# Performance work log

Hardware: AMD Instinct MI355X
Metric: run time of the kernel (lower is better)

The kernel has to match this reference:

```python
import jax, jax.numpy as jnp
import numpy as np

D_MODEL = 1024
NUM_HEADS = 16
HEAD_DIM = D_MODEL // NUM_HEADS


def setup_inputs() -> dict:
    key = jax.random.key(0)
    ks = jax.random.split(key, 9)
    B, S = 2, 2048
    s = 1.0 / np.sqrt(D_MODEL)
    inp = {
        "x": jax.random.normal(ks[0], (B, S, D_MODEL), dtype=jnp.float32),
        "Wq": jax.random.normal(ks[1], (D_MODEL, D_MODEL), dtype=jnp.float32) * s,
        "bq": jnp.zeros((D_MODEL,), dtype=jnp.float32),
        "Wk": jax.random.normal(ks[2], (D_MODEL, D_MODEL), dtype=jnp.float32) * s,
        "bk": jnp.zeros((D_MODEL,), dtype=jnp.float32),
        "Wv": jax.random.normal(ks[3], (D_MODEL, D_MODEL), dtype=jnp.float32) * s,
        "bv": jnp.zeros((D_MODEL,), dtype=jnp.float32),
        "Wo": jax.random.normal(ks[4], (D_MODEL, D_MODEL), dtype=jnp.float32) * s,
        "bo": jnp.zeros((D_MODEL,), dtype=jnp.float32),
    }
    return inp


def _rope(x, seq_len):
    # x: [B, H, S, Dh]; rotate-half RoPE with base 10000
    dh = x.shape[-1]
    inv_freq = 1.0 / (10000.0 ** (jnp.arange(0, dh, 2, dtype=jnp.float32) / dh))
    t = jnp.arange(seq_len, dtype=jnp.float32)
    freqs = jnp.einsum("i,j->ij", t, inv_freq)          # [S, Dh/2]
    emb = jnp.concatenate([freqs, freqs], axis=-1)        # [S, Dh]
    cos = jnp.cos(emb)[None, None, :, :]
    sin = jnp.sin(emb)[None, None, :, :]
    x1, x2 = jnp.split(x, 2, axis=-1)
    rot = jnp.concatenate([-x2, x1], axis=-1)
    return x * cos + rot * sin


def reference(x, Wq, bq, Wk, bk, Wv, bv, Wo, bo):
    B, S, _ = x.shape
    H, Dh = NUM_HEADS, HEAD_DIM

    def proj(W, b):
        y = x @ W.T + b                                   # [B, S, D]
        return y.reshape(B, S, H, Dh).transpose(0, 2, 1, 3)  # [B, H, S, Dh]

    q = _rope(proj(Wq, bq), S)
    k = _rope(proj(Wk, bk), S)
    v = proj(Wv, bv)

    scores = jnp.einsum("bhqd,bhkd->bhqk", q, k) / jnp.sqrt(jnp.float32(Dh))
    causal = jnp.triu(jnp.ones((S, S), dtype=bool), k=1)  # True above diag -> masked
    scores = jnp.where(causal[None, None], -jnp.inf, scores)
    attn = jax.nn.softmax(scores, axis=-1)
    out = jnp.einsum("bhqk,bhkd->bhqd", attn, v)          # [B, H, S, Dh]
    out = out.transpose(0, 2, 1, 3).reshape(B, S, H * Dh)
    return out @ Wo.T + bo
```

## Files before the change

### kernel.cpp

```cpp
#include <hip/hip_runtime.h>
#include <math.h>

typedef __bf16 bf16_t;
typedef bf16_t bf16x8 __attribute__((ext_vector_type(8)));
typedef float f32x4 __attribute__((ext_vector_type(4)));

#define S_LEN 2048
#define NHEAD 16
#define DHEAD 64
#define DMODEL 1024
#define BATCH 2

__device__ __forceinline__ float bf2f(unsigned short u) {
    unsigned int x = ((unsigned int)u) << 16;
    return __builtin_bit_cast(float, x);
}
__device__ __forceinline__ unsigned short f2bf(float f) {
    unsigned int x = __builtin_bit_cast(unsigned int, f);
    x += 0x7fffu + ((x >> 16) & 1u);
    return (unsigned short)(x >> 16);
}

__device__ __forceinline__ void glds16(const void* g, void* l) {
    __builtin_amdgcn_global_load_lds(
        (__attribute__((address_space(1))) void*)g,
        (__attribute__((address_space(3))) void*)l,
        16, 0, 0);
}

#define SCALE2 0.1803368801f

__global__ __launch_bounds__(256) void cvt_kernel(
    const float* __restrict__ x,  const float* __restrict__ wq,
    const float* __restrict__ wk, const float* __restrict__ wv,
    const float* __restrict__ wo,
    unsigned short* __restrict__ xb,  unsigned short* __restrict__ wqb,
    unsigned short* __restrict__ wkb, unsigned short* __restrict__ wvb,
    unsigned short* __restrict__ wob)
{
    const int y = blockIdx.y;
    const float* s = (y == 0) ? x : (y == 1) ? wq : (y == 2) ? wk : (y == 3) ? wv : wo;
    unsigned short* d = (y == 0) ? xb : (y == 1) ? wqb : (y == 2) ? wkb : (y == 3) ? wvb : wob;
    const int n4 = (y == 0) ? (1 << 20) : (1 << 18);
    const int i = blockIdx.x * 256 + threadIdx.x;
    if (i < n4) {
        float4 v = ((const float4*)s)[i];
        ushort4 o;
        o.x = f2bf(v.x); o.y = f2bf(v.y); o.z = f2bf(v.z); o.w = f2bf(v.w);
        ((ushort4*)d)[i] = o;
    }
}

__global__ __launch_bounds__(256) void rope_table_kernel(float2* __restrict__ tab)
{
    const int gid = blockIdx.x * 256 + threadIdx.x;
    const int s = gid >> 5, d = gid & 31;
    const float freq = exp2f(-0.4152410119f * (float)d);
    const float ang = (float)s * freq;
    tab[gid] = make_float2(cosf(ang), sinf(ang));
}

__global__ __launch_bounds__(256, 2) void qkv_gemm_kernel(
    const unsigned short* __restrict__ xb,
    const unsigned short* __restrict__ wqb, const unsigned short* __restrict__ wkb,
    const unsigned short* __restrict__ wvb,
    const float* __restrict__ bq, const float* __restrict__ bk, const float* __restrict__ bv,
    const float2* __restrict__ tab,
    unsigned short* __restrict__ Qr, unsigned short* __restrict__ Kr,
    unsigned short* __restrict__ VT)
{
    __shared__ __align__(16) unsigned short As[128 * 32];
    __shared__ __align__(16) unsigned short Bs[128 * 32];

    const int which = blockIdx.x >> 3;
    const int bn = (blockIdx.x & 7) * 128;
    const int bm = blockIdx.y * 128;
    const unsigned short* W = (which == 0) ? wqb : (which == 1) ? wkb : wvb;
    const float* bias       = (which == 0) ? bq  : (which == 1) ? bk  : bv;

    const int tid  = threadIdx.x;
    const int lane = tid & 63;
    const int w    = tid >> 6;
    const int quad = lane >> 4;
    const int l16  = lane & 15;
    const int wm   = (w >> 1) * 64;
    const int wn   = (w & 1) * 64;

    f32x4 acc[4][4];
#pragma unroll
    for (int i = 0; i < 4; ++i)
#pragma unroll
        for (int j = 0; j < 4; ++j)
            acc[i][j] = f32x4{0.f, 0.f, 0.f, 0.f};

    const int r0 = tid >> 2, c0 = (tid & 3) * 8;
    const unsigned short* ga0 = xb + (size_t)(bm + r0) * DMODEL + c0;
    const unsigned short* ga1 = ga0 + (size_t)64 * DMODEL;
    const unsigned short* gb0 = W  + (size_t)(bn + r0) * DMODEL + c0;
    const unsigned short* gb1 = gb0 + (size_t)64 * DMODEL;
    unsigned short* la0 = As + tid * 8;
    unsigned short* la1 = As + (tid + 256) * 8;
    unsigned short* lb0 = Bs + tid * 8;
    unsigned short* lb1 = Bs + (tid + 256) * 8;

    for (int k0 = 0; k0 < DMODEL; k0 += 32) {
        glds16(ga0 + k0, la0);
        glds16(ga1 + k0, la1);
        glds16(gb0 + k0, lb0);
        glds16(gb1 + k0, lb1);
        __syncthreads();

        bf16x8 aF[4], bF[4];
#pragma unroll
        for (int t = 0; t < 4; ++t) {
            aF[t] = *(const bf16x8*)(&As[(wm + t * 16 + l16) * 32 + quad * 8]);
            bF[t] = *(const bf16x8*)(&Bs[(wn + t * 16 + l16) * 32 + quad * 8]);
        }
#pragma unroll
        for (int mt = 0; mt < 4; ++mt)
#pragma unroll
            for (int nt = 0; nt < 4; ++nt)
                acc[mt][nt] = __builtin_amdgcn_mfma_f32_16x16x32_bf16(
                    aF[mt], bF[nt], acc[mt][nt], 0, 0, 0);
        __syncthreads();
    }

    if (which < 2) {
        unsigned short* Y = (which == 0) ? Qr : Kr;
        const float qscale = (which == 0) ? SCALE2 : 1.0f;
#pragma unroll
        for (int mt = 0; mt < 4; ++mt) {
            const int row0 = bm + wm + mt * 16 + quad * 4;
#pragma unroll
            for (int nt = 0; nt < 2; ++nt) {
                const int d   = nt * 16 + l16;
                const int col = bn + wn + nt * 16 + l16;
                const float b1 = bias[col];
                const float b2 = bias[col + 32];
#pragma unroll
                for (int r = 0; r < 4; ++r) {
                    const int row = row0 + r;
                    const int s = row & (S_LEN - 1);
                    const float2 cs = tab[s * 32 + d];
                    const float x1 = acc[mt][nt][r] + b1;
                    const float x2 = acc[mt][nt + 2][r] + b2;
                    Y[(size_t)row * DMODEL + col]      = f2bf((x1 * cs.x - x2 * cs.y) * qscale);
                    Y[(size_t)row * DMODEL + col + 32] = f2bf((x2 * cs.x + x1 * cs.y) * qscale);
                }
            }
        }
    } else {
#pragma unroll
        for (int mt = 0; mt < 4; ++mt) {
            const int row0 = bm + wm + mt * 16 + quad * 4;
            const int bb = row0 >> 11, s0 = row0 & (S_LEN - 1);
            const int h = (bn + wn) >> 6;
#pragma unroll
            for (int nt = 0; nt < 4; ++nt) {
                const int d = nt * 16 + l16;
                const float bv2 = bias[bn + wn + nt * 16 + l16];
                unsigned short pk[4];
#pragma unroll
                for (int r = 0; r < 4; ++r)
                    pk[r] = f2bf(acc[mt][nt][r] + bv2);
                *(uint2*)(&VT[((size_t)(bb * NHEAD + h) * DHEAD + d) * S_LEN + s0]) =
                    *(const uint2*)pk;
            }
        }
    }
}

#define VSTR 136

__global__ __launch_bounds__(512, 4) void attn_kernel(
    const unsigned short* __restrict__ Q, const unsigned short* __restrict__ K,
    const unsigned short* __restrict__ VT, unsigned short* __restrict__ O)
{
    const int j  = blockIdx.x;
    const int u  = j & 255;
    const int b  = j >> 8;
    const int m  = u & 15;
    int qt = (m & 1) ? (m >> 1) : (15 - (m >> 1));
    if (b) qt = 15 - qt;
    const int h  = u >> 4;

    const int tid  = threadIdx.x;
    const int w    = tid >> 6;
    const int lane = tid & 63;
    const int quad = lane >> 4;
    const int l16  = lane & 15;

    __shared__ __align__(16) unsigned short Ks[128 * 64];
    __shared__ __align__(16) unsigned short Vt[64 * 128];
    __shared__ __align__(16) unsigned short Pb[8 * 16 * VSTR];

    const int q0 = qt * 128;
    const unsigned short* Qb = Q  + (size_t)b * S_LEN * DMODEL + h * DHEAD;
    const unsigned short* Kb = K  + (size_t)b * S_LEN * DMODEL + h * DHEAD;
    const unsigned short* Vh = VT + ((size_t)(b * NHEAD + h)) * DHEAD * S_LEN;

    const int qrow = q0 + w * 16 + l16;
    const bf16x8 qf0 = *(const bf16x8*)(Qb + (size_t)qrow * DMODEL + quad * 8);
    const bf16x8 qf1 = *(const bf16x8*)(Qb + (size_t)qrow * DMODEL + 32 + quad * 8);

    f32x4 o[4];
#pragma unroll
    for (int i = 0; i < 4; ++i) o[i] = f32x4{0.f, 0.f, 0.f, 0.f};
    float l_i[4] = {0.f, 0.f, 0.f, 0.f};

    const int nkt = qt + 1;
    unsigned short* Pw = &Pb[w * 16 * VSTR];

    for (int kt = 0; kt < nkt; ++kt) {
#pragma unroll
        for (int i = 0; i < 2; ++i) {
            const int ck = tid + i * 512;
            const int krow = ck >> 3, kc = ck & 7;
            glds16(Kb + (size_t)(kt * 128 + krow) * DMODEL + ((kc ^ (krow & 7)) * 8),
                   Ks + ck * 8);
            const int vrow = ck >> 4, vc = ck & 15;
            glds16(Vh + (size_t)vrow * S_LEN + kt * 128 + ((vc ^ (vrow & 15)) * 8),
                   Vt + ck * 8);
        }
        __syncthreads();

        const bool diag = (kt == nkt - 1);
        const int ntmax = diag ? ((w & ~1) + 2) : 8;
        const int cmax  = ntmax >> 1;

        f32x4 sc[8];
#pragma unroll
        for (int nt = 0; nt < 8; ++nt) {
            if (nt >= ntmax) break;
            const int row = nt * 16 + l16;
            const bf16x8 kf0 = *(const bf16x8*)(&Ks[row * 64 + ((quad ^ (l16 & 7)) * 8)]);
            const bf16x8 kf1 = *(const bf16x8*)(&Ks[row * 64 + (((4 + quad) ^ (l16 & 7)) * 8)]);
            f32x4 a = f32x4{0.f, 0.f, 0.f, 0.f};
            a = __builtin_amdgcn_mfma_f32_16x16x32_bf16(qf0, kf0, a, 0, 0, 0);
            a = __builtin_amdgcn_mfma_f32_16x16x32_bf16(qf1, kf1, a, 0, 0, 0);
            sc[nt] = a;
        }

        if (diag) {
            const int qpos0 = q0 + w * 16 + quad * 4;
#pragma unroll
            for (int nt = 0; nt < 8; ++nt) {
                if (nt >= ntmax) break;
                const int kpos = kt * 128 + nt * 16 + l16;
#pragma unroll
                for (int r = 0; r < 4; ++r)
                    if (kpos > qpos0 + r) sc[nt][r] = -INFINITY;
            }
        }

#pragma unroll
        for (int nt = 0; nt < 8; ++nt) {
            if (nt >= ntmax) break;
#pragma unroll
            for (int r = 0; r < 4; ++r) {
                const float e = exp2f(sc[nt][r]);
                sc[nt][r] = e;
                l_i[r] += e;
            }
        }

#pragma unroll
        for (int nt = 0; nt < 8; ++nt) {
            if (nt >= ntmax) break;
#pragma unroll
            for (int r = 0; r < 4; ++r)
                Pw[(quad * 4 + r) * VSTR + nt * 16 + l16] = f2bf(sc[nt][r]);
        }

        bf16x8 pA[4];
#pragma unroll
        for (int c = 0; c < 4; ++c) {
            if (c >= cmax) break;
            pA[c] = *(const bf16x8*)(&Pw[l16 * VSTR + c * 32 + quad * 8]);
        }
#pragma unroll
        for (int nt = 0; nt < 4; ++nt) {
            const int row = nt * 16 + l16;
#pragma unroll
            for (int c = 0; c < 4; ++c) {
                if (c >= cmax) break;
                const bf16x8 vF = *(const bf16x8*)(&Vt[row * 128 + (((c * 4 + quad) ^ l16) * 8)]);
                o[nt] = __builtin_amdgcn_mfma_f32_16x16x32_bf16(pA[c], vF, o[nt], 0, 0, 0);
            }
        }
        __syncthreads();
    }

    float linv[4];
#pragma unroll
    for (int r = 0; r < 4; ++r) {
        float rs = l_i[r];
#pragma unroll
        for (int msk = 1; msk < 16; msk <<= 1)
            rs += __shfl_xor(rs, msk);
        linv[r] = 1.0f / rs;
    }
    const int spos0 = q0 + w * 16 + quad * 4;
#pragma unroll
    for (int nt = 0; nt < 4; ++nt)
#pragma unroll
        for (int r = 0; r < 4; ++r) {
            const float val = o[nt][r] * linv[r];
            O[((size_t)b * S_LEN + spos0 + r) * DMODEL + h * DHEAD + nt * 16 + l16] = f2bf(val);
        }
}

__global__ __launch_bounds__(256, 2) void outproj_kernel(
    const unsigned short* __restrict__ A, const unsigned short* __restrict__ W,
    const float* __restrict__ bias, float* __restrict__ C)
{
    __shared__ __align__(16) unsigned short As[64 * 32];
    __shared__ __align__(16) unsigned short Bs[128 * 32];

    const int tid  = threadIdx.x;
    const int lane = tid & 63;
    const int w    = tid >> 6;
    const int quad = lane >> 4;
    const int l16  = lane & 15;
    const int wm   = (w >> 1) * 32;
    const int wn   = (w & 1) * 64;
    const int bm   = blockIdx.y * 64;
    const int bn   = blockIdx.x * 128;

    f32x4 acc[2][4];
#pragma unroll
    for (int i = 0; i < 2; ++i)
#pragma unroll
        for (int j = 0; j < 4; ++j)
            acc[i][j] = f32x4{0.f, 0.f, 0.f, 0.f};

    const int r0 = tid >> 2, c0 = (tid & 3) * 8;
    const unsigned short* ga  = A + (size_t)(bm + r0) * DMODEL + c0;
    const unsigned short* gb0 = W + (size_t)(bn + r0) * DMODEL + c0;
    const unsigned short* gb1 = gb0 + (size_t)64 * DMODEL;
    unsigned short* la  = As + tid * 8;
    unsigned short* lb0 = Bs + tid * 8;
    unsigned short* lb1 = Bs + (tid + 256) * 8;

    for (int k0 = 0; k0 < DMODEL; k0 += 32) {
        glds16(ga + k0, la);
        glds16(gb0 + k0, lb0);
        glds16(gb1 + k0, lb1);
        __syncthreads();

        bf16x8 aF[2], bF[4];
#pragma unroll
        for (int t = 0; t < 2; ++t)
            aF[t] = *(const bf16x8*)(&As[(wm + t * 16 + l16) * 32 + quad * 8]);
#pragma unroll
        for (int t = 0; t < 4; ++t)
            bF[t] = *(const bf16x8*)(&Bs[(wn + t * 16 + l16) * 32 + quad * 8]);
#pragma unroll
        for (int mt = 0; mt < 2; ++mt)
#pragma unroll
            for (int nt = 0; nt < 4; ++nt)
                acc[mt][nt] = __builtin_amdgcn_mfma_f32_16x16x32_bf16(
                    aF[mt], bF[nt], acc[mt][nt], 0, 0, 0);
        __syncthreads();
    }

#pragma unroll
    for (int mt = 0; mt < 2; ++mt) {
        const int row0 = bm + wm + mt * 16 + quad * 4;
#pragma unroll
        for (int nt = 0; nt < 4; ++nt) {
            const int col = bn + wn + nt * 16 + l16;
            const float bv = bias[col];
#pragma unroll
            for (int r = 0; r < 4; ++r)
                C[(size_t)(row0 + r) * DMODEL + col] = acc[mt][nt][r] + bv;
        }
    }
}

extern "C" void kernel_launch(void* const* d_in, const int* in_sizes, int n_in,
                              void* d_out, int out_size, void* d_ws, size_t ws_size,
                              hipStream_t stream) {
    const float* x  = (const float*)d_in[0];
    const float* Wq = (const float*)d_in[1];
    const float* bq = (const float*)d_in[2];
    const float* Wk = (const float*)d_in[3];
    const float* bk = (const float*)d_in[4];
    const float* Wv = (const float*)d_in[5];
    const float* bv = (const float*)d_in[6];
    const float* Wo = (const float*)d_in[7];
    const float* bo = (const float*)d_in[8];
    float* out = (float*)d_out;

    char* ws = (char*)d_ws;
    const size_t MB = 1 << 20;
    unsigned short* xb  = (unsigned short*)(ws);
    unsigned short* wqb = (unsigned short*)(ws + 8  * MB);
    unsigned short* wkb = (unsigned short*)(ws + 10 * MB);
    unsigned short* wvb = (unsigned short*)(ws + 12 * MB);
    unsigned short* wob = (unsigned short*)(ws + 14 * MB);
    float2*         tab = (float2*)       (ws + 16 * MB);
    unsigned short* Qr  = (unsigned short*)(ws + 17 * MB);
    unsigned short* Kr  = (unsigned short*)(ws + 25 * MB);
    unsigned short* VT  = (unsigned short*)(ws + 33 * MB);
    unsigned short* AO  = (unsigned short*)(ws + 41 * MB);

    const int M = BATCH * S_LEN;

    cvt_kernel<<<dim3(4096, 5), 256, 0, stream>>>(
        x, Wq, Wk, Wv, Wo, xb, wqb, wkb, wvb, wob);

    rope_table_kernel<<<256, 256, 0, stream>>>(tab);

    qkv_gemm_kernel<<<dim3(24, M / 128), 256, 0, stream>>>(
        xb, wqb, wkb, wvb, bq, bk, bv, tab, Qr, Kr, VT);

    attn_kernel<<<dim3(512), 512, 0, stream>>>(Qr, Kr, VT, AO);

    outproj_kernel<<<dim3(DMODEL / 128, M / 64), 256, 0, stream>>>(AO, wob, bo, out);
}
```

Baseline: 198.3 us.

## Split causal attention along KV into chunks and add a combine kernel

The attention kernel now processes at most four KV tiles per block, so the grid grows from 512 to 1280 blocks. Long query tiles are spread over several blocks, which should cut the tail caused by causal imbalance, where the last query tile needs sixteen KV tiles and the first needs one. Each block writes unnormalized fp32 partial outputs and row sums to workspace, and a new combine kernel adds them, normalizes, and writes the bf16 result. The cost is an extra launch and extra global traffic for the fp32 partials. Summing partials directly is only correct because the softmax does not track a per-block running max.

```diff
diff --git a/kernel.cpp b/kernel.cpp
--- a/kernel.cpp
+++ b/kernel.cpp
@@ -171,18 +171,25 @@
 }
 
 #define VSTR 136
+#define CHUNK 4
 
 __global__ __launch_bounds__(512, 4) void attn_kernel(
     const unsigned short* __restrict__ Q, const unsigned short* __restrict__ K,
-    const unsigned short* __restrict__ VT, unsigned short* __restrict__ O)
-{
-    const int j  = blockIdx.x;
-    const int u  = j & 255;
-    const int b  = j >> 8;
-    const int m  = u & 15;
-    int qt = (m & 1) ? (m >> 1) : (15 - (m >> 1));
-    if (b) qt = 15 - qt;
-    const int h  = u >> 4;
+    const unsigned short* __restrict__ VT,
+    float* __restrict__ Opart, float* __restrict__ Lpart)
+{
+    const int j   = blockIdx.x;
+    const int bh  = j / 40;
+    const int cid = 39 - (j - bh * 40);
+    const int b   = bh >> 4, h = bh & 15;
+    int g, rel;
+    if (cid < 4)       { g = 0; rel = cid; }
+    else if (cid < 12) { g = 1; rel = cid - 4; }
+    else if (cid < 24) { g = 2; rel = cid - 12; }
+    else               { g = 3; rel = cid - 24; }
+    const int qt = 4 * g + rel / (g + 1);
+    const int cs = rel - (rel / (g + 1)) * (g + 1);
+    const int slot = bh * 40 + cid;
 
     const int tid  = threadIdx.x;
     const int w    = tid >> 6;
@@ -208,10 +215,11 @@
     for (int i = 0; i < 4; ++i) o[i] = f32x4{0.f, 0.f, 0.f, 0.f};
     float l_i[4] = {0.f, 0.f, 0.f, 0.f};
 
-    const int nkt = qt + 1;
+    const int k0t  = cs * CHUNK;
+    const int kend = (k0t + CHUNK < qt + 1) ? (k0t + CHUNK) : (qt + 1);
     unsigned short* Pw = &Pb[w * 16 * VSTR];
 
-    for (int kt = 0; kt < nkt; ++kt) {
+    for (int kt = k0t; kt < kend; ++kt) {
 #pragma unroll
         for (int i = 0; i < 2; ++i) {
             const int ck = tid + i * 512;
@@ -224,7 +232,7 @@
         }
         __syncthreads();
 
-        const bool diag = (kt == nkt - 1);
+        const bool diag = (kt == qt);
         const int ntmax = diag ? ((w & ~1) + 2) : 8;
         const int cmax  = ntmax >> 1;
 
@@ -291,23 +299,53 @@
         __syncthreads();
     }
 
-    float linv[4];
+    float* Op = Opart + (size_t)slot * (128 * 64);
+    float* Lp = Lpart + slot * 128;
+    const int row0 = w * 16 + quad * 4;
 #pragma unroll
     for (int r = 0; r < 4; ++r) {
         float rs = l_i[r];
 #pragma unroll
         for (int msk = 1; msk < 16; msk <<= 1)
             rs += __shfl_xor(rs, msk);
-        linv[r] = 1.0f / rs;
-    }
-    const int spos0 = q0 + w * 16 + quad * 4;
+        if (l16 == 0) Lp[row0 + r] = rs;
+    }
 #pragma unroll
     for (int nt = 0; nt < 4; ++nt)
 #pragma unroll
-        for (int r = 0; r < 4; ++r) {
-            const float val = o[nt][r] * linv[r];
-            O[((size_t)b * S_LEN + spos0 + r) * DMODEL + h * DHEAD + nt * 16 + l16] = f2bf(val);
-        }
+        for (int r = 0; r < 4; ++r)
+            Op[(row0 + r) * 64 + nt * 16 + l16] = o[nt][r];
+}
+
+__global__ __launch_bounds__(256) void attn_combine_kernel(
+    const float* __restrict__ Opart, const float* __restrict__ Lpart,
+    unsigned short* __restrict__ AO)
+{
+    const int bid = blockIdx.x;
+    const int b = bid >> 8, rem = bid & 255, h = rem >> 4, qt = rem & 15;
+    const int g = qt >> 2, rr = qt & 3;
+    const int off = (g + 1) * (2 * g + rr);
+    const int nc  = g + 1;
+    const int s0  = (b * NHEAD + h) * 40 + off;
+    const int t   = threadIdx.x;
+
+#pragma unroll
+    for (int jj = 0; jj < 8; ++jj) {
+        const int idx = jj * 1024 + t * 4;
+        const int row = idx >> 6, dh = idx & 63;
+        float4 acc = make_float4(0.f, 0.f, 0.f, 0.f);
+        float l = 0.f;
+        for (int c = 0; c < nc; ++c) {
+            const float4 p = *(const float4*)(Opart + (size_t)(s0 + c) * 8192 + idx);
+            acc.x += p.x; acc.y += p.y; acc.z += p.z; acc.w += p.w;
+            l += Lpart[(s0 + c) * 128 + row];
+        }
+        const float linv = 1.0f / l;
+        ushort4 o;
+        o.x = f2bf(acc.x * linv); o.y = f2bf(acc.y * linv);
+        o.z = f2bf(acc.z * linv); o.w = f2bf(acc.w * linv);
+        *(ushort4*)(AO + ((size_t)(b * S_LEN + qt * 128 + row)) * DMODEL + h * DHEAD + dh) = o;
+    }
 }
 
 __global__ __launch_bounds__(256, 2) void outproj_kernel(
@@ -404,6 +442,8 @@
     unsigned short* Kr  = (unsigned short*)(ws + 25 * MB);
     unsigned short* VT  = (unsigned short*)(ws + 33 * MB);
     unsigned short* AO  = (unsigned short*)(ws + 41 * MB);
+    float*          Opart = (float*)      (ws + 49 * MB);
+    float*          Lpart = (float*)      (ws + 90 * MB);
 
     const int M = BATCH * S_LEN;
 
@@ -415,7 +455,9 @@
     qkv_gemm_kernel<<<dim3(24, M / 128), 256, 0, stream>>>(
         xb, wqb, wkb, wvb, bq, bk, bv, tab, Qr, Kr, VT);
 
-    attn_kernel<<<dim3(512), 512, 0, stream>>>(Qr, Kr, VT, AO);
+    attn_kernel<<<dim3(1280), 512, 0, stream>>>(Qr, Kr, VT, Opart, Lpart);
+
+    attn_combine_kernel<<<dim3(512), 256, 0, stream>>>(Opart, Lpart, AO);
 
     outproj_kernel<<<dim3(DMODEL / 128, M / 64), 256, 0, stream>>>(AO, wob, bo, out);
 }
```

After: 227.2 us. 14.6% more time.

## Pair causal query tiles per block and double-buffer K/V loads in attention

Applied to the files above, without the earlier changes.

Each attention block now handles two complementary query tiles (15-m and m), so every block does a balanced 17 key-tile steps, and the grid is halved to 256 blocks. K and V tiles are double-buffered in LDS, with the next tile's async global-to-LDS loads issued before the current tile's compute and gated by explicit vmcnt waits and raw barriers. This targets causal load imbalance and exposed load latency. In exchange it doubles K/V LDS use, drops the occupancy hint, and leaves fewer blocks than the previous 512 to fill the GPU's compute units.

```diff
diff --git a/kernel.cpp b/kernel.cpp
--- a/kernel.cpp
+++ b/kernel.cpp
@@ -171,18 +171,18 @@
 }
 
 #define VSTR 136
-
-__global__ __launch_bounds__(512, 4) void attn_kernel(
+#define NSTG 17
+
+__global__ __launch_bounds__(512) void attn_kernel(
     const unsigned short* __restrict__ Q, const unsigned short* __restrict__ K,
     const unsigned short* __restrict__ VT, unsigned short* __restrict__ O)
 {
-    const int j  = blockIdx.x;
-    const int u  = j & 255;
-    const int b  = j >> 8;
-    const int m  = u & 15;
-    int qt = (m & 1) ? (m >> 1) : (15 - (m >> 1));
-    if (b) qt = 15 - qt;
-    const int h  = u >> 4;
+    const int j   = blockIdx.x;
+    const int bh  = j >> 3;
+    const int m   = j & 7;
+    const int b   = bh >> 4, h = bh & 15;
+    const int qtA = 15 - m;
+    const int nA  = qtA + 1;
 
     const int tid  = threadIdx.x;
     const int w    = tid >> 6;
@@ -190,41 +190,66 @@
     const int quad = lane >> 4;
     const int l16  = lane & 15;
 
-    __shared__ __align__(16) unsigned short Ks[128 * 64];
-    __shared__ __align__(16) unsigned short Vt[64 * 128];
+    __shared__ __align__(16) unsigned short Ks[2][128 * 64];
+    __shared__ __align__(16) unsigned short Vt[2][64 * 128];
     __shared__ __align__(16) unsigned short Pb[8 * 16 * VSTR];
 
-    const int q0 = qt * 128;
     const unsigned short* Qb = Q  + (size_t)b * S_LEN * DMODEL + h * DHEAD;
     const unsigned short* Kb = K  + (size_t)b * S_LEN * DMODEL + h * DHEAD;
     const unsigned short* Vh = VT + ((size_t)(b * NHEAD + h)) * DHEAD * S_LEN;
 
-    const int qrow = q0 + w * 16 + l16;
-    const bf16x8 qf0 = *(const bf16x8*)(Qb + (size_t)qrow * DMODEL + quad * 8);
-    const bf16x8 qf1 = *(const bf16x8*)(Qb + (size_t)qrow * DMODEL + 32 + quad * 8);
+    const int rA = qtA * 128 + w * 16 + l16;
+    const int rB = m   * 128 + w * 16 + l16;
+    const bf16x8 qfA0 = *(const bf16x8*)(Qb + (size_t)rA * DMODEL + quad * 8);
+    const bf16x8 qfA1 = *(const bf16x8*)(Qb + (size_t)rA * DMODEL + 32 + quad * 8);
+    const bf16x8 qfB0 = *(const bf16x8*)(Qb + (size_t)rB * DMODEL + quad * 8);
+    const bf16x8 qfB1 = *(const bf16x8*)(Qb + (size_t)rB * DMODEL + 32 + quad * 8);
 
     f32x4 o[4];
 #pragma unroll
     for (int i = 0; i < 4; ++i) o[i] = f32x4{0.f, 0.f, 0.f, 0.f};
     float l_i[4] = {0.f, 0.f, 0.f, 0.f};
 
-    const int nkt = qt + 1;
     unsigned short* Pw = &Pb[w * 16 * VSTR];
 
-    for (int kt = 0; kt < nkt; ++kt) {
-#pragma unroll
-        for (int i = 0; i < 2; ++i) {
-            const int ck = tid + i * 512;
-            const int krow = ck >> 3, kc = ck & 7;
-            glds16(Kb + (size_t)(kt * 128 + krow) * DMODEL + ((kc ^ (krow & 7)) * 8),
-                   Ks + ck * 8);
-            const int vrow = ck >> 4, vc = ck & 15;
-            glds16(Vh + (size_t)vrow * S_LEN + kt * 128 + ((vc ^ (vrow & 15)) * 8),
-                   Vt + ck * 8);
-        }
-        __syncthreads();
-
-        const bool diag = (kt == nkt - 1);
+#define STAGE(bs, kt_) do {                                                        \
+        _Pragma("unroll")                                                          \
+        for (int i_ = 0; i_ < 2; ++i_) {                                           \
+            const int ck = tid + i_ * 512;                                         \
+            const int krow = ck >> 3, kc = ck & 7;                                 \
+            glds16(Kb + (size_t)((kt_) * 128 + krow) * DMODEL + ((kc ^ (krow & 7)) * 8), \
+                   &Ks[bs][ck * 8]);                                               \
+            const int vrow = ck >> 4, vc = ck & 15;                                \
+            glds16(Vh + (size_t)vrow * S_LEN + (kt_) * 128 + ((vc ^ (vrow & 15)) * 8), \
+                   &Vt[bs][ck * 8]);                                               \
+        }                                                                          \
+    } while (0)
+
+    STAGE(0, 0);
+
+    for (int st = 0; st < NSTG; ++st) {
+        const int cur = st & 1;
+
+        if (st + 1 < NSTG) {
+            const int kt2 = (st + 1 < nA) ? (st + 1) : (st + 1 - nA);
+            STAGE(cur ^ 1, kt2);
+            if (st == nA) {
+                asm volatile("s_waitcnt vmcnt(20)" ::: "memory");
+            } else {
+                asm volatile("s_waitcnt vmcnt(4)" ::: "memory");
+            }
+        } else {
+            asm volatile("s_waitcnt vmcnt(0)" ::: "memory");
+        }
+        __builtin_amdgcn_s_barrier();
+
+        const int inA = (st < nA) ? 1 : 0;
+        const int qt  = inA ? qtA : m;
+        const int kt  = inA ? st : st - nA;
+        const bf16x8 qv0 = inA ? qfA0 : qfB0;
+        const bf16x8 qv1 = inA ? qfA1 : qfB1;
+
+        const bool diag = (kt == qt);
         const int ntmax = diag ? ((w & ~1) + 2) : 8;
         const int cmax  = ntmax >> 1;
 
@@ -233,16 +258,16 @@
         for (int nt = 0; nt < 8; ++nt) {
             if (nt >= ntmax) break;
             const int row = nt * 16 + l16;
-            const bf16x8 kf0 = *(const bf16x8*)(&Ks[row * 64 + ((quad ^ (l16 & 7)) * 8)]);
-            const bf16x8 kf1 = *(const bf16x8*)(&Ks[row * 64 + (((4 + quad) ^ (l16 & 7)) * 8)]);
+            const bf16x8 kf0 = *(const bf16x8*)(&Ks[cur][row * 64 + ((quad ^ (l16 & 7)) * 8)]);
+            const bf16x8 kf1 = *(const bf16x8*)(&Ks[cur][row * 64 + (((4 + quad) ^ (l16 & 7)) * 8)]);
             f32x4 a = f32x4{0.f, 0.f, 0.f, 0.f};
-            a = __builtin_amdgcn_mfma_f32_16x16x32_bf16(qf0, kf0, a, 0, 0, 0);
-            a = __builtin_amdgcn_mfma_f32_16x16x32_bf16(qf1, kf1, a, 0, 0, 0);
+            a = __builtin_amdgcn_mfma_f32_16x16x32_bf16(qv0, kf0, a, 0, 0, 0);
+            a = __builtin_amdgcn_mfma_f32_16x16x32_bf16(qv1, kf1, a, 0, 0, 0);
             sc[nt] = a;
         }
 
         if (diag) {
-            const int qpos0 = q0 + w * 16 + quad * 4;
+            const int qpos0 = qt * 128 + w * 16 + quad * 4;
 #pragma unroll
             for (int nt = 0; nt < 8; ++nt) {
                 if (nt >= ntmax) break;
@@ -284,30 +309,59 @@
 #pragma unroll
             for (int c = 0; c < 4; ++c) {
                 if (c >= cmax) break;
-                const bf16x8 vF = *(const bf16x8*)(&Vt[row * 128 + (((c * 4 + quad) ^ l16) * 8)]);
+                const bf16x8 vF = *(const bf16x8*)(&Vt[cur][row * 128 + (((c * 4 + quad) ^ l16) * 8)]);
                 o[nt] = __builtin_amdgcn_mfma_f32_16x16x32_bf16(pA[c], vF, o[nt], 0, 0, 0);
             }
         }
-        __syncthreads();
-    }
-
-    float linv[4];
-#pragma unroll
-    for (int r = 0; r < 4; ++r) {
-        float rs = l_i[r];
-#pragma unroll
-        for (int msk = 1; msk < 16; msk <<= 1)
-            rs += __shfl_xor(rs, msk);
-        linv[r] = 1.0f / rs;
-    }
-    const int spos0 = q0 + w * 16 + quad * 4;
-#pragma unroll
-    for (int nt = 0; nt < 4; ++nt)
+
+        asm volatile("s_waitcnt lgkmcnt(0)" ::: "memory");
+        __builtin_amdgcn_s_barrier();
+
+        if (st == nA - 1) {
+            float linv[4];
+#pragma unroll
+            for (int r = 0; r < 4; ++r) {
+                float rs = l_i[r];
+#pragma unroll
+                for (int msk = 1; msk < 16; msk <<= 1)
+                    rs += __shfl_xor(rs, msk);
+                linv[r] = 1.0f / rs;
+            }
+            const int spos0 = qtA * 128 + w * 16 + quad * 4;
+#pragma unroll
+            for (int nt = 0; nt < 4; ++nt)
+#pragma unroll
+                for (int r = 0; r < 4; ++r) {
+                    const float val = o[nt][r] * linv[r];
+                    O[((size_t)b * S_LEN + spos0 + r) * DMODEL + h * DHEAD + nt * 16 + l16] = f2bf(val);
+                }
+#pragma unroll
+            for (int i = 0; i < 4; ++i) o[i] = f32x4{0.f, 0.f, 0.f, 0.f};
+#pragma unroll
+            for (int r = 0; r < 4; ++r) l_i[r] = 0.f;
+        }
+    }
+#undef STAGE
+
+    {
+        float linv[4];
 #pragma unroll
         for (int r = 0; r < 4; ++r) {
-            const float val = o[nt][r] * linv[r];
-            O[((size_t)b * S_LEN + spos0 + r) * DMODEL + h * DHEAD + nt * 16 + l16] = f2bf(val);
-        }
+            float rs = l_i[r];
+#pragma unroll
+            for (int msk = 1; msk < 16; msk <<= 1)
+                rs += __shfl_xor(rs, msk);
+            linv[r] = 1.0f / rs;
+        }
+        const int spos0 = m * 128 + w * 16 + quad * 4;
+#pragma unroll
+        for (int nt = 0; nt < 4; ++nt)
+#pragma unroll
+            for (int r = 0; r < 4; ++r) {
+                const float val = o[nt][r] * linv[r];
+                O[((size_t)b * S_LEN + spos0 + r) * DMODEL + h * DHEAD + nt * 16 + l16] = f2bf(val);
+            }
+    }
 }
 
 __global__ __launch_bounds__(256, 2) void outproj_kernel(
@@ -415,7 +469,7 @@
     qkv_gemm_kernel<<<dim3(24, M / 128), 256, 0, stream>>>(
         xb, wqb, wkb, wvb, bq, bk, bv, tab, Qr, Kr, VT);
 
-    attn_kernel<<<dim3(512), 512, 0, stream>>>(Qr, Kr, VT, AO);
+    attn_kernel<<<dim3(256), 512, 0, stream>>>(Qr, Kr, VT, AO);
 
     outproj_kernel<<<dim3(DMODEL / 128, M / 64), 256, 0, stream>>>(AO, wob, bo, out);
 }
```

After: 206.2 us. +4.0%, slower.

## Double-buffer K/V tiles and build P operand in registers via lane shuffles

Applied to the files above, without the earlier changes.

The attention kernel now double-buffers the K and V tiles in LDS, prefetching the next tile with async global-to-LDS loads while the current one is computed, and uses explicit vmcnt waits with raw barriers. The QK MFMA operands are swapped so the score tile is transposed, which lets the P matrix be packed to bf16 with v_cvt_pk_bf16_f32 and rearranged through cross-lane shuffles instead of a round trip through an LDS scratch buffer. The block-to-tile mapping is also reordered to interleave heads with long and short causal tiles. This trades LDS traffic and load latency for extra shuffle and select instructions, and the doubled K/V buffers may change occupancy.

```diff
diff --git a/kernel.cpp b/kernel.cpp
--- a/kernel.cpp
+++ b/kernel.cpp
@@ -4,6 +4,7 @@
 typedef __bf16 bf16_t;
 typedef bf16_t bf16x8 __attribute__((ext_vector_type(8)));
 typedef float f32x4 __attribute__((ext_vector_type(4)));
+typedef unsigned int u32x4 __attribute__((ext_vector_type(4)));
 
 #define S_LEN 2048
 #define NHEAD 16
@@ -170,19 +171,15 @@
     }
 }
 
-#define VSTR 136
-
 __global__ __launch_bounds__(512, 4) void attn_kernel(
     const unsigned short* __restrict__ Q, const unsigned short* __restrict__ K,
     const unsigned short* __restrict__ VT, unsigned short* __restrict__ O)
 {
     const int j  = blockIdx.x;
-    const int u  = j & 255;
-    const int b  = j >> 8;
-    const int m  = u & 15;
-    int qt = (m & 1) ? (m >> 1) : (15 - (m >> 1));
-    if (b) qt = 15 - qt;
-    const int h  = u >> 4;
+    const int bh = j & 31;
+    const int qs = j >> 5;
+    const int b  = bh >> 4, h = bh & 15;
+    const int qt = (qs < 8) ? (15 - qs) : (qs - 8);
 
     const int tid  = threadIdx.x;
     const int w    = tid >> 6;
@@ -190,9 +187,8 @@
     const int quad = lane >> 4;
     const int l16  = lane & 15;
 
-    __shared__ __align__(16) unsigned short Ks[128 * 64];
-    __shared__ __align__(16) unsigned short Vt[64 * 128];
-    __shared__ __align__(16) unsigned short Pb[8 * 16 * VSTR];
+    __shared__ __align__(16) unsigned short Ks[2][128 * 64];
+    __shared__ __align__(16) unsigned short Vt[2][64 * 128];
 
     const int q0 = qt * 128;
     const unsigned short* Qb = Q  + (size_t)b * S_LEN * DMODEL + h * DHEAD;
@@ -206,25 +202,37 @@
     f32x4 o[4];
 #pragma unroll
     for (int i = 0; i < 4; ++i) o[i] = f32x4{0.f, 0.f, 0.f, 0.f};
-    float l_i[4] = {0.f, 0.f, 0.f, 0.f};
+    float l_acc = 0.f;
 
     const int nkt = qt + 1;
-    unsigned short* Pw = &Pb[w * 16 * VSTR];
+
+#define STAGE(bs, kt_) do {                                                        \
+        _Pragma("unroll")                                                          \
+        for (int i_ = 0; i_ < 2; ++i_) {                                           \
+            const int ck = tid + i_ * 512;                                         \
+            const int krow = ck >> 3, kc = ck & 7;                                 \
+            glds16(Kb + (size_t)((kt_) * 128 + krow) * DMODEL + ((kc ^ (krow & 7)) * 8), \
+                   &Ks[bs][ck * 8]);                                               \
+            const int vrow = ck >> 4, vc = ck & 15;                                \
+            glds16(Vh + (size_t)vrow * S_LEN + (kt_) * 128 + ((vc ^ (vrow & 15)) * 8), \
+                   &Vt[bs][ck * 8]);                                               \
+        }                                                                          \
+    } while (0)
+
+    STAGE(0, 0);
 
     for (int kt = 0; kt < nkt; ++kt) {
-#pragma unroll
-        for (int i = 0; i < 2; ++i) {
-            const int ck = tid + i * 512;
-            const int krow = ck >> 3, kc = ck & 7;
-            glds16(Kb + (size_t)(kt * 128 + krow) * DMODEL + ((kc ^ (krow & 7)) * 8),
-                   Ks + ck * 8);
-            const int vrow = ck >> 4, vc = ck & 15;
-            glds16(Vh + (size_t)vrow * S_LEN + kt * 128 + ((vc ^ (vrow & 15)) * 8),
-                   Vt + ck * 8);
-        }
-        __syncthreads();
-
-        const bool diag = (kt == nkt - 1);
+        const int cur = kt & 1;
+
+        if (kt + 1 < nkt) {
+            STAGE(cur ^ 1, kt + 1);
+            asm volatile("s_waitcnt vmcnt(4)" ::: "memory");
+        } else {
+            asm volatile("s_waitcnt vmcnt(0)" ::: "memory");
+        }
+        __builtin_amdgcn_s_barrier();
+
+        const bool diag = (kt == qt);
         const int ntmax = diag ? ((w & ~1) + 2) : 8;
         const int cmax  = ntmax >> 1;
 
@@ -233,23 +241,22 @@
         for (int nt = 0; nt < 8; ++nt) {
             if (nt >= ntmax) break;
             const int row = nt * 16 + l16;
-            const bf16x8 kf0 = *(const bf16x8*)(&Ks[row * 64 + ((quad ^ (l16 & 7)) * 8)]);
-            const bf16x8 kf1 = *(const bf16x8*)(&Ks[row * 64 + (((4 + quad) ^ (l16 & 7)) * 8)]);
+            const bf16x8 kf0 = *(const bf16x8*)(&Ks[cur][row * 64 + ((quad ^ (l16 & 7)) * 8)]);
+            const bf16x8 kf1 = *(const bf16x8*)(&Ks[cur][row * 64 + (((4 + quad) ^ (l16 & 7)) * 8)]);
             f32x4 a = f32x4{0.f, 0.f, 0.f, 0.f};
-            a = __builtin_amdgcn_mfma_f32_16x16x32_bf16(qf0, kf0, a, 0, 0, 0);
-            a = __builtin_amdgcn_mfma_f32_16x16x32_bf16(qf1, kf1, a, 0, 0, 0);
+            a = __builtin_amdgcn_mfma_f32_16x16x32_bf16(kf0, qf0, a, 0, 0, 0);
+            a = __builtin_amdgcn_mfma_f32_16x16x32_bf16(kf1, qf1, a, 0, 0, 0);
             sc[nt] = a;
         }
 
         if (diag) {
-            const int qpos0 = q0 + w * 16 + quad * 4;
+            const int thr = q0 + w * 16 + l16 - kt * 128 - quad * 4;
 #pragma unroll
             for (int nt = 0; nt < 8; ++nt) {
                 if (nt >= ntmax) break;
-                const int kpos = kt * 128 + nt * 16 + l16;
 #pragma unroll
                 for (int r = 0; r < 4; ++r)
-                    if (kpos > qpos0 + r) sc[nt][r] = -INFINITY;
+                    if (nt * 16 + r > thr) sc[nt][r] = -INFINITY;
             }
         }
 
@@ -260,54 +267,68 @@
             for (int r = 0; r < 4; ++r) {
                 const float e = exp2f(sc[nt][r]);
                 sc[nt][r] = e;
-                l_i[r] += e;
-            }
-        }
-
-#pragma unroll
-        for (int nt = 0; nt < 8; ++nt) {
-            if (nt >= ntmax) break;
-#pragma unroll
-            for (int r = 0; r < 4; ++r)
-                Pw[(quad * 4 + r) * VSTR + nt * 16 + l16] = f2bf(sc[nt][r]);
+                l_acc += e;
+            }
         }
 
         bf16x8 pA[4];
+        const bool qlo = (quad < 2);
 #pragma unroll
         for (int c = 0; c < 4; ++c) {
             if (c >= cmax) break;
-            pA[c] = *(const bf16x8*)(&Pw[l16 * VSTR + c * 32 + quad * 8]);
-        }
+            unsigned int s0, s1, t0, t1;
+            asm("v_cvt_pk_bf16_f32 %0, %1, %2" : "=v"(s0) : "v"(sc[2*c][0]),   "v"(sc[2*c][1]));
+            asm("v_cvt_pk_bf16_f32 %0, %1, %2" : "=v"(s1) : "v"(sc[2*c][2]),   "v"(sc[2*c][3]));
+            asm("v_cvt_pk_bf16_f32 %0, %1, %2" : "=v"(t0) : "v"(sc[2*c+1][0]), "v"(sc[2*c+1][1]));
+            asm("v_cvt_pk_bf16_f32 %0, %1, %2" : "=v"(t1) : "v"(sc[2*c+1][2]), "v"(sc[2*c+1][3]));
+            const unsigned int m0 = qlo ? s0 : t0, m1 = qlo ? s1 : t1;
+            const unsigned int n0 = qlo ? t0 : s0, n1 = qlo ? t1 : s1;
+            const unsigned int X0 = __shfl_xor(m0, 16), X1 = __shfl_xor(m1, 16);
+            const unsigned int A0 = __shfl_xor(n0, 32), A1 = __shfl_xor(n1, 32);
+            const unsigned int B0 = __shfl_xor(n0, 48), B1 = __shfl_xor(n1, 48);
+            u32x4 aw;
+            aw[0] = qlo ? (quad == 0 ? m0 : B0) : (quad == 2 ? A0 : X0);
+            aw[1] = qlo ? (quad == 0 ? m1 : B1) : (quad == 2 ? A1 : X1);
+            aw[2] = qlo ? (quad == 0 ? X0 : A0) : (quad == 2 ? B0 : m0);
+            aw[3] = qlo ? (quad == 0 ? X1 : A1) : (quad == 2 ? B1 : m1);
+            pA[c] = __builtin_bit_cast(bf16x8, aw);
+        }
+
 #pragma unroll
         for (int nt = 0; nt < 4; ++nt) {
             const int row = nt * 16 + l16;
 #pragma unroll
             for (int c = 0; c < 4; ++c) {
                 if (c >= cmax) break;
-                const bf16x8 vF = *(const bf16x8*)(&Vt[row * 128 + (((c * 4 + quad) ^ l16) * 8)]);
+                const bf16x8 vF = *(const bf16x8*)(&Vt[cur][row * 128 + (((c * 4 + quad) ^ l16) * 8)]);
                 o[nt] = __builtin_amdgcn_mfma_f32_16x16x32_bf16(pA[c], vF, o[nt], 0, 0, 0);
             }
         }
-        __syncthreads();
-    }
-
-    float linv[4];
-#pragma unroll
-    for (int r = 0; r < 4; ++r) {
-        float rs = l_i[r];
-#pragma unroll
-        for (int msk = 1; msk < 16; msk <<= 1)
-            rs += __shfl_xor(rs, msk);
-        linv[r] = 1.0f / rs;
-    }
-    const int spos0 = q0 + w * 16 + quad * 4;
-#pragma unroll
-    for (int nt = 0; nt < 4; ++nt)
-#pragma unroll
-        for (int r = 0; r < 4; ++r) {
-            const float val = o[nt][r] * linv[r];
-            O[((size_t)b * S_LEN + spos0 + r) * DMODEL + h * DHEAD + nt * 16 + l16] = f2bf(val);
-        }
+
+        asm volatile("s_waitcnt lgkmcnt(0)" ::: "memory");
+        __builtin_amdgcn_s_barrier();
+    }
+#undef STAGE
+
+    {
+        float rs = l_acc;
+        rs += __shfl_xor(rs, 16);
+        rs += __shfl_xor(rs, 32);
+        const float linv_row = 1.0f / rs;
+        float linv[4];
+#pragma unroll
+        for (int r = 0; r < 4; ++r)
+            linv[r] = __shfl(linv_row, quad * 4 + r);
+
+        const int spos0 = q0 + w * 16 + quad * 4;
+#pragma unroll
+        for (int nt = 0; nt < 4; ++nt)
+#pragma unroll
+            for (int r = 0; r < 4; ++r) {
+                const float val = o[nt][r] * linv[r];
+                O[((size_t)b * S_LEN + spos0 + r) * DMODEL + h * DHEAD + nt * 16 + l16] = f2bf(val);
+            }
+    }
 }
 
 __global__ __launch_bounds__(256, 2) void outproj_kernel(
```

Result: no change. 196.6 us (-0.8%).
